# Optimization experiments

Hardware: AMD Instinct MI355X
Metric: run time of the kernel (lower is better)

The kernel has to match this reference:

```python
import jax, jax.numpy as jnp
import numpy as np

GAMMA = 1.0
N_EXPERTS = 16
K = 8                      # number of trees (units of every Dense)
DEPTH = 4                  # log2(N_EXPERTS)
B, D_IN, D_OUT = 8192, 1024, 1024


def smoothstep(v):
    # 0 if v<=-g/2 ; 1 if v>=g/2 ; -2/g^3 v^3 + 3/(2g) v + 0.5 otherwise
    g = GAMMA
    poly = (-2.0 / g**3) * v**3 + (3.0 / (2.0 * g)) * v + 0.5
    return jnp.where(v <= -g / 2, 0.0, jnp.where(v >= g / 2, 1.0, poly))


def setup_inputs() -> dict:
    key = jax.random.key(0)
    ks = jax.random.split(key, 7)
    f = jax.random.normal(ks[0], (B, D_OUT, N_EXPERTS), jnp.float32)   # stacked experts
    x = jax.random.normal(ks[1], (B, D_IN), jnp.float32)               # routing inputs
    permutation_weights = jax.random.uniform(ks[2], (K, N_EXPERTS, N_EXPERTS), jnp.float32)
    zlo, zhi = -GAMMA / 100, GAMMA / 100                               # z_initializer range
    Wz = jax.random.uniform(ks[3], (N_EXPERTS - 1, D_IN, K), jnp.float32, zlo, zhi)
    bz = jax.random.uniform(ks[4], (N_EXPERTS - 1, K), jnp.float32, zlo, zhi)
    Ww = jax.random.uniform(ks[5], (N_EXPERTS, D_IN, K), jnp.float32)  # w_initializer U(0,1)
    bw = jax.random.uniform(ks[6], (N_EXPERTS, K), jnp.float32)
    return {"f": f, "x": x, "permutation_weights": permutation_weights,
            "Wz": Wz, "bz": bz, "Ww": Ww, "bw": bw}


def reference(f, x, permutation_weights, Wz, bz, Ww, bw):
    b = x.shape[0]
    # selector activations for all internal nodes (BFS order): [B, N_EXPERTS-1, K]
    s = smoothstep(jnp.einsum('bd,ndk->bnk', x, Wz) + bz)
    # propagate path probabilities level by level down the complete binary tree
    prob = jnp.ones((b, 1, K), x.dtype)
    for level in range(DEPTH):
        start = 2**level - 1
        p = s[:, start:start + 2**level, :]               # [B, 2^level, K]
        # left child gets prob*p, right child gets prob*(1-p)
        prob = jnp.stack([prob * p, prob * (1.0 - p)], axis=2).reshape(b, 2**(level + 1), K)
    # leaf dense outputs: [B, N_EXPERTS, K]
    a = jnp.einsum('bd,ndk->bnk', x, Ww) + bw
    log_prob = jnp.where(prob <= 0.0, jnp.finfo(jnp.float32).min, jnp.log(prob + 1e-8))
    s_bj = jnp.swapaxes(a + log_prob, 1, 2)               # [B, K, N_EXPERTS] (leaf order)
    g = jax.nn.softmax(s_bj.reshape(b, K * N_EXPERTS), axis=-1)
    g = g.reshape(b, 1, K, N_EXPERTS)                     # [B, 1, K, N]
    g_perm = jnp.einsum('bijk,jkl->bijl', g, permutation_weights)
    g_perm = jnp.sum(g_perm, axis=2, keepdims=True)       # [B, 1, 1, N]
    g_perm = g_perm / jnp.sum(g_perm, axis=-1, keepdims=True)
    # y = sum_n f[:, :, n] * g[:, n]  -> [B, D_OUT]
    y = jnp.einsum('bdn,bn->bd', f, g_perm[:, 0, 0, :])
    return y
```

## Files before the change

### kernel.cpp

```cpp
#include <hip/hip_runtime.h>
#include <math.h>

#define B_ROWS 8192
#define D_IN 1024
#define D_OUT 1024
#define NEXP 16
#define KDIM 8
#define NCOL 256

typedef __attribute__((ext_vector_type(8))) short bf16x8;
typedef __attribute__((ext_vector_type(4))) float f32x4;

__device__ __forceinline__ unsigned short f2bf_rne(float v) {
    unsigned u = __float_as_uint(v);
    u += 0x7fffu + ((u >> 16) & 1u);
    return (unsigned short)(u >> 16);
}
__device__ __forceinline__ float bf2f(unsigned short h) {
    return __uint_as_float(((unsigned)h) << 16);
}

__global__ __launch_bounds__(256) void wt_pack_kernel(const float* __restrict__ Wz,
                                                      const float* __restrict__ Ww,
                                                      float* __restrict__ WtT) {
    const int c = blockIdx.x;
    for (int d = threadIdx.x; d < D_IN; d += 256) {
        float v = 0.0f;
        if (c < 120) {
            const int n = c >> 3, k = c & 7;
            v = Wz[n * (D_IN * KDIM) + d * KDIM + k];
        } else if (c < 248) {
            const int cc = c - 120;
            const int n = cc >> 3, k = cc & 7;
            v = Ww[n * (D_IN * KDIM) + d * KDIM + k];
        }
        WtT[c * D_IN + d] = v;
    }
}

#define BM 64
#define BN 64
#define KB 32

__global__ __launch_bounds__(256) void gemm_kernel(const float* __restrict__ x,
                                                   const float* __restrict__ WtT,
                                                   float* __restrict__ ZA) {
    __shared__ bf16x8 XH[256], XL[256], WH[256], WL[256];

    const int tid = threadIdx.x;
    const int wave = tid >> 6;
    const int lane = tid & 63;
    const int rowBase = blockIdx.x * BM;
    const int colBase = blockIdx.y * BN;

    const int sRow = tid >> 2;
    const int sKg = tid & 3;
    const float* xg = x + (size_t)(rowBase + sRow) * D_IN + sKg * 8;
    const float* wg = WtT + (size_t)(colBase + sRow) * D_IN + sKg * 8;
    const int sUnit = ((sRow >> 4) << 6) | (sKg << 4) | (sRow & 15);

    f32x4 acc[4];
#pragma unroll
    for (int ct = 0; ct < 4; ++ct)
#pragma unroll
        for (int q = 0; q < 4; ++q) acc[ct][q] = 0.0f;

    float4 px0 = *(const float4*)(xg + 0);
    float4 px1 = *(const float4*)(xg + 4);
    float4 pw0 = *(const float4*)(wg + 0);
    float4 pw1 = *(const float4*)(wg + 4);

    for (int kk = 0; kk < D_IN; kk += KB) {
        const float xv[8] = {px0.x, px0.y, px0.z, px0.w, px1.x, px1.y, px1.z, px1.w};
        const float wv[8] = {pw0.x, pw0.y, pw0.z, pw0.w, pw1.x, pw1.y, pw1.z, pw1.w};
        bf16x8 xh, xl, wh, wl;
#pragma unroll
        for (int i = 0; i < 8; ++i) {
            unsigned short h = f2bf_rne(xv[i]);
            xh[i] = (short)h;
            xl[i] = (short)f2bf_rne(xv[i] - bf2f(h));
            h = f2bf_rne(wv[i]);
            wh[i] = (short)h;
            wl[i] = (short)f2bf_rne(wv[i] - bf2f(h));
        }
        XH[sUnit] = xh; XL[sUnit] = xl; WH[sUnit] = wh; WL[sUnit] = wl;
        __syncthreads();

        if (kk + KB < D_IN) {
            px0 = *(const float4*)(xg + kk + KB);
            px1 = *(const float4*)(xg + kk + KB + 4);
            pw0 = *(const float4*)(wg + kk + KB);
            pw1 = *(const float4*)(wg + kk + KB + 4);
        }

        const bf16x8 ah = XH[(wave << 6) | lane];
        const bf16x8 al = XL[(wave << 6) | lane];
#pragma unroll
        for (int ct = 0; ct < 4; ++ct) {
            const bf16x8 bh = WH[(ct << 6) | lane];
            const bf16x8 bl = WL[(ct << 6) | lane];
            acc[ct] = __builtin_amdgcn_mfma_f32_16x16x32_bf16(ah, bh, acc[ct], 0, 0, 0);
            acc[ct] = __builtin_amdgcn_mfma_f32_16x16x32_bf16(ah, bl, acc[ct], 0, 0, 0);
            acc[ct] = __builtin_amdgcn_mfma_f32_16x16x32_bf16(al, bh, acc[ct], 0, 0, 0);
        }
        __syncthreads();
    }

    const int cRow = rowBase + wave * 16 + ((lane >> 4) << 2);
    const int cCol = colBase + (lane & 15);
#pragma unroll
    for (int ct = 0; ct < 4; ++ct)
#pragma unroll
        for (int q = 0; q < 4; ++q)
            ZA[(size_t)(cRow + q) * NCOL + cCol + ct * 16] = acc[ct][q];
}

__global__ __launch_bounds__(128) void gate_kernel(const float* __restrict__ ZA,
                                                   const float* __restrict__ bz,
                                                   const float* __restrict__ bw,
                                                   const float* __restrict__ perm,
                                                   float* __restrict__ wout) {
    __shared__ float red[128];
    __shared__ float u[128];

    const int b = blockIdx.x;
    const int tid = threadIdx.x;
    const int kk = tid >> 4;
    const int n = tid & 15;

    const float* za = ZA + b * NCOL;

    float prob = 1.0f;
#pragma unroll
    for (int L = 0; L < 4; ++L) {
        const int node = (1 << L) - 1 + (n >> (4 - L));
        const int bit = (n >> (3 - L)) & 1;
        const float v = za[node * 8 + kk] + bz[node * 8 + kk];
        float p;
        if (v <= -0.5f) p = 0.0f;
        else if (v >= 0.5f) p = 1.0f;
        else p = fmaf(-2.0f * v * v, v, fmaf(1.5f, v, 0.5f));
        prob *= bit ? (1.0f - p) : p;
    }

    const float a = za[120 + n * 8 + kk] + bw[n * 8 + kk];
    const float logit = (prob <= 0.0f) ? -3.4e38f : (a + logf(prob + 1e-8f));

    red[tid] = logit;
    __syncthreads();
#pragma unroll
    for (int s = 64; s > 0; s >>= 1) {
        if (tid < s) red[tid] = fmaxf(red[tid], red[tid + s]);
        __syncthreads();
    }
    const float mx = red[0];
    __syncthreads();

    u[tid] = expf(logit - mx);
    __syncthreads();

    const int l = tid & 15;
    const int chunk = tid >> 4;
    float partial = 0.0f;
#pragma unroll
    for (int e0 = 0; e0 < 16; ++e0) {
        const int e = chunk * 16 + e0;
        partial += u[e] * perm[(e >> 4) * 256 + (e & 15) * 16 + l];
    }
    red[tid] = partial;
    __syncthreads();
#pragma unroll
    for (int s = 64; s >= 16; s >>= 1) {
        if (tid < s) red[tid] += red[tid + s];
        __syncthreads();
    }
    if (tid < 16) {
        float tot = 0.0f;
#pragma unroll
        for (int l2 = 0; l2 < 16; ++l2) tot += red[l2];
        wout[b * NEXP + tid] = red[tid] / tot;
    }
}

__global__ __launch_bounds__(256) void out_kernel(const float* __restrict__ f,
                                                  const float* __restrict__ w,
                                                  float* __restrict__ y) {
    __shared__ float ws_[16];
    const int b = blockIdx.x >> 2;
    const int d = ((blockIdx.x & 3) << 8) + threadIdx.x;
    if (threadIdx.x < 16) ws_[threadIdx.x] = w[b * NEXP + threadIdx.x];
    __syncthreads();

    const long idx = (long)b * D_OUT + d;
    const float4* f4 = (const float4*)(f + idx * NEXP);
    const float4 a0 = f4[0];
    const float4 a1 = f4[1];
    const float4 a2 = f4[2];
    const float4 a3 = f4[3];

    float r = a0.x * ws_[0] + a0.y * ws_[1] + a0.z * ws_[2] + a0.w * ws_[3]
            + a1.x * ws_[4] + a1.y * ws_[5] + a1.z * ws_[6] + a1.w * ws_[7]
            + a2.x * ws_[8] + a2.y * ws_[9] + a2.z * ws_[10] + a2.w * ws_[11]
            + a3.x * ws_[12] + a3.y * ws_[13] + a3.z * ws_[14] + a3.w * ws_[15];
    y[idx] = r;
}

extern "C" void kernel_launch(void* const* d_in, const int* in_sizes, int n_in,
                              void* d_out, int out_size, void* d_ws, size_t ws_size,
                              hipStream_t stream) {
    const float* f = (const float*)d_in[0];
    const float* x = (const float*)d_in[1];
    const float* perm = (const float*)d_in[2];
    const float* Wz = (const float*)d_in[3];
    const float* bz = (const float*)d_in[4];
    const float* Ww = (const float*)d_in[5];
    const float* bw = (const float*)d_in[6];
    float* y = (float*)d_out;

    float* WtT = (float*)d_ws;
    float* ZA = WtT + NCOL * D_IN;
    float* Wexp = ZA + (size_t)B_ROWS * NCOL;

    wt_pack_kernel<<<dim3(NCOL), dim3(256), 0, stream>>>(Wz, Ww, WtT);
    gemm_kernel<<<dim3(B_ROWS / BM, NCOL / BN), dim3(256), 0, stream>>>(x, WtT, ZA);
    gate_kernel<<<dim3(B_ROWS), dim3(128), 0, stream>>>(ZA, bz, bw, perm, Wexp);
    out_kernel<<<dim3(B_ROWS * 4), dim3(256), 0, stream>>>(f, Wexp, y);
}
```

Measured before the change: 763.5 us.

## Fuse routing GEMM with gate softmax and prepack weights into bf16 hi/lo

Merges the routing GEMM and the per-row gate computation into a single kernel where each block handles 16 rows across all 256 columns, keeping logits in shared memory and using wave shuffles for the softmax reductions. Weights are pre-split into bf16 high/low fragments in MFMA layout by a packing kernel, so the main loop loads them directly from global memory without LDS staging or barriers. This removes the intermediate ZA buffer round trip, one kernel launch, and the heavily synchronised gate kernel. In exchange the GEMM loses shared-memory reuse of weights and runs fewer, larger blocks, relying on L2 for weight reads.

```diff
diff --git a/kernel.cpp b/kernel.cpp
--- a/kernel.cpp
+++ b/kernel.cpp
@@ -5,7 +5,6 @@
 #define D_IN 1024
 #define D_OUT 1024
 #define NEXP 16
-#define KDIM 8
 #define NCOL 256
 
 typedef __attribute__((ext_vector_type(8))) short bf16x8;
@@ -20,44 +19,68 @@
     return __uint_as_float(((unsigned)h) << 16);
 }
 
-__global__ __launch_bounds__(256) void wt_pack_kernel(const float* __restrict__ Wz,
-                                                      const float* __restrict__ Ww,
-                                                      float* __restrict__ WtT) {
-    const int c = blockIdx.x;
-    for (int d = threadIdx.x; d < D_IN; d += 256) {
-        float v = 0.0f;
-        if (c < 120) {
-            const int n = c >> 3, k = c & 7;
-            v = Wz[n * (D_IN * KDIM) + d * KDIM + k];
-        } else if (c < 248) {
-            const int cc = c - 120;
-            const int n = cc >> 3, k = cc & 7;
-            v = Ww[n * (D_IN * KDIM) + d * KDIM + k];
-        }
-        WtT[c * D_IN + d] = v;
-    }
-}
-
-#define BM 64
-#define BN 64
-#define KB 32
-
-__global__ __launch_bounds__(256) void gemm_kernel(const float* __restrict__ x,
-                                                   const float* __restrict__ WtT,
-                                                   float* __restrict__ ZA) {
-    __shared__ bf16x8 XH[256], XL[256], WH[256], WL[256];
+__global__ __launch_bounds__(256) void wpack_kernel(const float* __restrict__ Wz,
+                                                    const float* __restrict__ Ww,
+                                                    bf16x8* __restrict__ WH,
+                                                    bf16x8* __restrict__ WL) {
+    const int U = blockIdx.x * 256 + threadIdx.x;
+    const int c15 = U & 15;
+    const int kg = (U >> 4) & 3;
+    const int cg = (U >> 6) & 15;
+    const int kc = U >> 10;
+    const int col = cg * 16 + c15;
+    const int d0 = kc * 32 + kg * 8;
+
+    const float* src = nullptr;
+    if (col < 120) {
+        const int n = col >> 3, k = col & 7;
+        src = Wz + n * (D_IN * 8) + k;
+    } else if (col < 248) {
+        const int c = col - 120;
+        const int n = c >> 3, k = c & 7;
+        src = Ww + n * (D_IN * 8) + k;
+    }
+    bf16x8 h, lo;
+#pragma unroll
+    for (int e = 0; e < 8; ++e) {
+        const float v = src ? src[(d0 + e) * 8] : 0.0f;
+        const unsigned short hh = f2bf_rne(v);
+        h[e] = (short)hh;
+        lo[e] = (short)f2bf_rne(v - bf2f(hh));
+    }
+    WH[U] = h;
+    WL[U] = lo;
+}
+
+__global__ __launch_bounds__(256, 2) void fused_kernel(const float* __restrict__ x,
+                                                       const bf16x8* __restrict__ WH,
+                                                       const bf16x8* __restrict__ WL,
+                                                       const float* __restrict__ perm,
+                                                       const float* __restrict__ bz,
+                                                       const float* __restrict__ bw,
+                                                       float* __restrict__ wout) {
+    __shared__ __align__(16) float ZAs[16][NCOL];
+    __shared__ float us[16][8][16];
+    __shared__ __align__(16) float permS[8 * 256];
+    __shared__ float bzS[120];
+    __shared__ float bwS[128];
 
     const int tid = threadIdx.x;
-    const int wave = tid >> 6;
-    const int lane = tid & 63;
-    const int rowBase = blockIdx.x * BM;
-    const int colBase = blockIdx.y * BN;
-
-    const int sRow = tid >> 2;
-    const int sKg = tid & 3;
-    const float* xg = x + (size_t)(rowBase + sRow) * D_IN + sKg * 8;
-    const float* wg = WtT + (size_t)(colBase + sRow) * D_IN + sKg * 8;
-    const int sUnit = ((sRow >> 4) << 6) | (sKg << 4) | (sRow & 15);
+    const int w = tid >> 6;
+    const int l = tid & 63;
+    const int rowBase = blockIdx.x * 16;
+    const int cgBase = w * 4;
+
+    {
+        const float4* p4 = (const float4*)perm;
+        float4* s4 = (float4*)permS;
+        s4[tid * 2 + 0] = p4[tid * 2 + 0];
+        s4[tid * 2 + 1] = p4[tid * 2 + 1];
+        if (tid < 120) bzS[tid] = bz[tid];
+        if (tid < 128) bwS[tid] = bw[tid];
+    }
+
+    const float* xg = x + (size_t)(rowBase + (l & 15)) * D_IN + ((l >> 4) << 3);
 
     f32x4 acc[4];
 #pragma unroll
@@ -65,121 +88,86 @@
 #pragma unroll
         for (int q = 0; q < 4; ++q) acc[ct][q] = 0.0f;
 
-    float4 px0 = *(const float4*)(xg + 0);
-    float4 px1 = *(const float4*)(xg + 4);
-    float4 pw0 = *(const float4*)(wg + 0);
-    float4 pw1 = *(const float4*)(wg + 4);
-
-    for (int kk = 0; kk < D_IN; kk += KB) {
-        const float xv[8] = {px0.x, px0.y, px0.z, px0.w, px1.x, px1.y, px1.z, px1.w};
-        const float wv[8] = {pw0.x, pw0.y, pw0.z, pw0.w, pw1.x, pw1.y, pw1.z, pw1.w};
-        bf16x8 xh, xl, wh, wl;
+#pragma unroll 4
+    for (int kc = 0; kc < 32; ++kc) {
+        bf16x8 bh[4], bl[4];
+#pragma unroll
+        for (int ct = 0; ct < 4; ++ct) {
+            const int u = (kc * 16 + cgBase + ct) * 64 + l;
+            bh[ct] = WH[u];
+            bl[ct] = WL[u];
+        }
+        const float4 xa = *(const float4*)(xg + kc * 32);
+        const float4 xb = *(const float4*)(xg + kc * 32 + 4);
+        const float xv[8] = {xa.x, xa.y, xa.z, xa.w, xb.x, xb.y, xb.z, xb.w};
+        bf16x8 ah, al;
 #pragma unroll
         for (int i = 0; i < 8; ++i) {
-            unsigned short h = f2bf_rne(xv[i]);
-            xh[i] = (short)h;
-            xl[i] = (short)f2bf_rne(xv[i] - bf2f(h));
-            h = f2bf_rne(wv[i]);
-            wh[i] = (short)h;
-            wl[i] = (short)f2bf_rne(wv[i] - bf2f(h));
-        }
-        XH[sUnit] = xh; XL[sUnit] = xl; WH[sUnit] = wh; WL[sUnit] = wl;
-        __syncthreads();
-
-        if (kk + KB < D_IN) {
-            px0 = *(const float4*)(xg + kk + KB);
-            px1 = *(const float4*)(xg + kk + KB + 4);
-            pw0 = *(const float4*)(wg + kk + KB);
-            pw1 = *(const float4*)(wg + kk + KB + 4);
-        }
-
-        const bf16x8 ah = XH[(wave << 6) | lane];
-        const bf16x8 al = XL[(wave << 6) | lane];
+            const unsigned short hh = f2bf_rne(xv[i]);
+            ah[i] = (short)hh;
+            al[i] = (short)f2bf_rne(xv[i] - bf2f(hh));
+        }
 #pragma unroll
         for (int ct = 0; ct < 4; ++ct) {
-            const bf16x8 bh = WH[(ct << 6) | lane];
-            const bf16x8 bl = WL[(ct << 6) | lane];
-            acc[ct] = __builtin_amdgcn_mfma_f32_16x16x32_bf16(ah, bh, acc[ct], 0, 0, 0);
-            acc[ct] = __builtin_amdgcn_mfma_f32_16x16x32_bf16(ah, bl, acc[ct], 0, 0, 0);
-            acc[ct] = __builtin_amdgcn_mfma_f32_16x16x32_bf16(al, bh, acc[ct], 0, 0, 0);
-        }
-        __syncthreads();
-    }
-
-    const int cRow = rowBase + wave * 16 + ((lane >> 4) << 2);
-    const int cCol = colBase + (lane & 15);
-#pragma unroll
-    for (int ct = 0; ct < 4; ++ct)
-#pragma unroll
-        for (int q = 0; q < 4; ++q)
-            ZA[(size_t)(cRow + q) * NCOL + cCol + ct * 16] = acc[ct][q];
-}
-
-__global__ __launch_bounds__(128) void gate_kernel(const float* __restrict__ ZA,
-                                                   const float* __restrict__ bz,
-                                                   const float* __restrict__ bw,
-                                                   const float* __restrict__ perm,
-                                                   float* __restrict__ wout) {
-    __shared__ float red[128];
-    __shared__ float u[128];
-
-    const int b = blockIdx.x;
-    const int tid = threadIdx.x;
-    const int kk = tid >> 4;
-    const int n = tid & 15;
-
-    const float* za = ZA + b * NCOL;
-
-    float prob = 1.0f;
-#pragma unroll
-    for (int L = 0; L < 4; ++L) {
-        const int node = (1 << L) - 1 + (n >> (4 - L));
-        const int bit = (n >> (3 - L)) & 1;
-        const float v = za[node * 8 + kk] + bz[node * 8 + kk];
-        float p;
-        if (v <= -0.5f) p = 0.0f;
-        else if (v >= 0.5f) p = 1.0f;
-        else p = fmaf(-2.0f * v * v, v, fmaf(1.5f, v, 0.5f));
-        prob *= bit ? (1.0f - p) : p;
-    }
-
-    const float a = za[120 + n * 8 + kk] + bw[n * 8 + kk];
-    const float logit = (prob <= 0.0f) ? -3.4e38f : (a + logf(prob + 1e-8f));
-
-    red[tid] = logit;
+            acc[ct] = __builtin_amdgcn_mfma_f32_16x16x32_bf16(ah, bh[ct], acc[ct], 0, 0, 0);
+            acc[ct] = __builtin_amdgcn_mfma_f32_16x16x32_bf16(ah, bl[ct], acc[ct], 0, 0, 0);
+            acc[ct] = __builtin_amdgcn_mfma_f32_16x16x32_bf16(al, bh[ct], acc[ct], 0, 0, 0);
+        }
+    }
+
+    {
+        const int r0 = (l >> 4) << 2;
+        const int c0 = l & 15;
+#pragma unroll
+        for (int ct = 0; ct < 4; ++ct) {
+            const int c = w * 64 + ct * 16 + c0;
+#pragma unroll
+            for (int q = 0; q < 4; ++q) ZAs[r0 + q][c] = acc[ct][q];
+        }
+    }
     __syncthreads();
-#pragma unroll
-    for (int s = 64; s > 0; s >>= 1) {
-        if (tid < s) red[tid] = fmaxf(red[tid], red[tid + s]);
-        __syncthreads();
-    }
-    const float mx = red[0];
+
+    const int r = tid >> 4;
+    const int g = tid & 15;
+
+    float logit[8];
+#pragma unroll
+    for (int j = 0; j < 8; ++j) {
+        float prob = 1.0f;
+#pragma unroll
+        for (int L = 0; L < 4; ++L) {
+            const int node = (1 << L) - 1 + (g >> (4 - L));
+            const int bit = (g >> (3 - L)) & 1;
+            const float v = ZAs[r][node * 8 + j] + bzS[node * 8 + j];
+            float p;
+            if (v <= -0.5f) p = 0.0f;
+            else if (v >= 0.5f) p = 1.0f;
+            else p = fmaf(-2.0f * v * v, v, fmaf(1.5f, v, 0.5f));
+            prob *= bit ? (1.0f - p) : p;
+        }
+        const float a = ZAs[r][120 + g * 8 + j] + bwS[g * 8 + j];
+        logit[j] = (prob <= 0.0f) ? -3.4e38f : (a + logf(prob + 1e-8f));
+    }
+    float mx = logit[0];
+#pragma unroll
+    for (int j = 1; j < 8; ++j) mx = fmaxf(mx, logit[j]);
+#pragma unroll
+    for (int m = 1; m < 16; m <<= 1) mx = fmaxf(mx, __shfl_xor(mx, m));
+#pragma unroll
+    for (int j = 0; j < 8; ++j) us[r][j][g] = expf(logit[j] - mx);
     __syncthreads();
 
-    u[tid] = expf(logit - mx);
-    __syncthreads();
-
-    const int l = tid & 15;
-    const int chunk = tid >> 4;
-    float partial = 0.0f;
-#pragma unroll
-    for (int e0 = 0; e0 < 16; ++e0) {
-        const int e = chunk * 16 + e0;
-        partial += u[e] * perm[(e >> 4) * 256 + (e & 15) * 16 + l];
-    }
-    red[tid] = partial;
-    __syncthreads();
-#pragma unroll
-    for (int s = 64; s >= 16; s >>= 1) {
-        if (tid < s) red[tid] += red[tid + s];
-        __syncthreads();
-    }
-    if (tid < 16) {
-        float tot = 0.0f;
-#pragma unroll
-        for (int l2 = 0; l2 < 16; ++l2) tot += red[l2];
-        wout[b * NEXP + tid] = red[tid] / tot;
-    }
+    float wsum = 0.0f;
+#pragma unroll
+    for (int j = 0; j < 8; ++j)
+#pragma unroll
+        for (int n = 0; n < 16; ++n)
+            wsum = fmaf(us[r][j][n], permS[j * 256 + n * 16 + g], wsum);
+
+    float tot = wsum;
+#pragma unroll
+    for (int m = 1; m < 16; m <<= 1) tot += __shfl_xor(tot, m);
+    wout[(rowBase + r) * NEXP + g] = wsum / tot;
 }
 
 __global__ __launch_bounds__(256) void out_kernel(const float* __restrict__ f,
@@ -217,12 +205,11 @@
     const float* bw = (const float*)d_in[6];
     float* y = (float*)d_out;
 
-    float* WtT = (float*)d_ws;
-    float* ZA = WtT + NCOL * D_IN;
-    float* Wexp = ZA + (size_t)B_ROWS * NCOL;
-
-    wt_pack_kernel<<<dim3(NCOL), dim3(256), 0, stream>>>(Wz, Ww, WtT);
-    gemm_kernel<<<dim3(B_ROWS / BM, NCOL / BN), dim3(256), 0, stream>>>(x, WtT, ZA);
-    gate_kernel<<<dim3(B_ROWS), dim3(128), 0, stream>>>(ZA, bz, bw, perm, Wexp);
+    bf16x8* WH = (bf16x8*)d_ws;
+    bf16x8* WL = WH + 32768;
+    float* Wexp = (float*)(WL + 32768);
+
+    wpack_kernel<<<dim3(128), dim3(256), 0, stream>>>(Wz, Ww, WH, WL);
+    fused_kernel<<<dim3(B_ROWS / 16), dim3(256), 0, stream>>>(x, WH, WL, perm, bz, bw, Wexp);
     out_kernel<<<dim3(B_ROWS * 4), dim3(256), 0, stream>>>(f, Wexp, y);
 }
```

New measurement: 749.1 us. No clear change (-1.9%).
